# Performance work log

Hardware: AMD Instinct MI355X
Metric: run time of the kernel (lower is better)

Reference implementation:

```python
import jax, jax.numpy as jnp
import numpy as np

B, L, T = 512, 512, 128
START, STOP = T - 2, T - 1   # tag_dict: '<START>'->126, '<STOP>'->127
NEG = -10000.0


def setup_inputs() -> dict:
    key = jax.random.key(0)
    k1, k2, k3, k4 = jax.random.split(key, 4)
    feats = jax.random.normal(k1, (B, L, T), dtype=jnp.float32)
    # learned transition matrix, initialized as in CRF.__init__
    trans = jax.random.normal(k2, (T, T), dtype=jnp.float32)
    trans = trans.at[START, :].set(NEG).at[:, STOP].set(NEG)
    tags = jax.random.randint(k3, (B, L), 0, T - 2)          # gold tags, no START/STOP
    lens = jax.random.randint(k4, (B,), 1, L + 1)            # actual lengths in [1, L]
    return {"feats": feats, "transitions": trans, "tags": tags, "lens": lens}


def _crf_loss(feats, transitions, tags, lens):
    Bn, Ln, Tn = feats.shape

    # ---- forward algorithm (log partition) ----
    init = jnp.full((Tn,), NEG, dtype=feats.dtype).at[START].set(0.0)
    fv0 = jnp.broadcast_to(init, (Bn, Tn))

    def step(fv, xs):
        emit, i = xs                                  # emit: [B, T]
        # tag_var[b, next, prev] = emit[b,next] + trans[next,prev] + fv[b,prev]
        tv = emit[:, :, None] + transitions[None, :, :] + fv[:, None, :]
        new = jax.scipy.special.logsumexp(tv, axis=2)  # [B, T]
        # freeze fv once past each sentence's length (== gathering at index lens)
        fv = jnp.where((i < lens)[:, None], new, fv)
        return fv, None

    fv, _ = jax.lax.scan(step, fv0, (jnp.swapaxes(feats, 0, 1), jnp.arange(Ln)))
    terminal = fv + transitions[START][None, :]       # matches original (uses START row)
    forward_score = jax.scipy.special.logsumexp(terminal, axis=1)  # [B]

    # ---- gold sentence score ----
    start_col = jnp.full((Bn, 1), START, dtype=tags.dtype)
    stop_col = jnp.full((Bn, 1), STOP, dtype=tags.dtype)
    pad_start = jnp.concatenate([start_col, tags], axis=1)   # [B, L+1]
    pad_stop = jnp.concatenate([tags, stop_col], axis=1)     # [B, L+1]
    pos = jnp.arange(Ln + 1)[None, :]
    pad_stop = jnp.where(pos >= lens[:, None], STOP, pad_stop)

    trans_terms = transitions[pad_stop, pad_start]           # [B, L+1]
    trans_sum = jnp.sum(jnp.where(pos <= lens[:, None], trans_terms, 0.0), axis=1)
    emit_terms = jnp.take_along_axis(feats, tags[:, :, None], axis=2)[..., 0]  # [B, L]
    emit_mask = jnp.arange(Ln)[None, :] < lens[:, None]
    emit_sum = jnp.sum(jnp.where(emit_mask, emit_terms, 0.0), axis=1)
    gold_score = trans_sum + emit_sum

    return jnp.mean(forward_score - gold_score)


def reference(feats, transitions, tags, lens):
    return _crf_loss(feats, transitions, tags, lens)
```

## Files before the change

### kernel.cpp

```cpp
#include <hip/hip_runtime.h>

#define Bsz 512
#define Lsz 512
#define Tsz 128
#define TAG_START 126
#define TAG_STOP 127
#define SPB 16
#define UPITCH 136

typedef __attribute__((ext_vector_type(8))) short short8;
typedef __attribute__((ext_vector_type(4))) float f32x4;

__device__ __forceinline__ void lds_barrier() {
  asm volatile("s_waitcnt lgkmcnt(0)\n\ts_barrier" ::: "memory");
}
__device__ __forceinline__ unsigned pack_bf16(float lo, float hi) {
  unsigned a = (__float_as_uint(lo) + 0x8000u) >> 16;
  unsigned b = (__float_as_uint(hi) + 0x8000u) & 0xFFFF0000u;
  return b | a;
}
__device__ __forceinline__ float bf16lo(unsigned d) { return __uint_as_float(d << 16); }
__device__ __forceinline__ float bf16hi(unsigned d) { return __uint_as_float(d & 0xFFFF0000u); }

__global__ __launch_bounds__(256) void crf_fwd_kernel(
    const float* __restrict__ feats, const float* __restrict__ trans,
    const int* __restrict__ tags, const int* __restrict__ lens,
    float* __restrict__ diff_out)
{
  __shared__ __align__(16) unsigned short u_lds[2][SPB][UPITCH];
  __shared__ float red[4][SPB];
  __shared__ float gold_sh[SPB];
  __shared__ int msh;

  const int g    = blockIdx.x;
  const int tid  = threadIdx.x;
  const int w    = tid >> 6;
  const int lane = tid & 63;
  const int q    = lane >> 4;
  const int s    = lane & 15;
  const int seq  = g * SPB + s;
  const int lenc = lens[seq];
  const int lim  = lenc - 1;

  if (tid == 0) msh = 1;
  __syncthreads();
  if (tid < SPB) atomicMax(&msh, lens[g * SPB + tid]);
  for (int i = tid; i < 2 * SPB * UPITCH; i += 256)
    ((unsigned short*)u_lds)[i] = 0;
  __syncthreads();
  const int maxlen = msh;
  if (tid < SPB) u_lds[0][tid][TAG_START] = 0x3F80;
  __syncthreads();

  short8 af[2][4];
  #pragma unroll
  for (int i = 0; i < 2; ++i) {
    const float* tr = trans + (size_t)((2 * w + i) * 16 + s) * Tsz + q * 8;
    #pragma unroll
    for (int c = 0; c < 4; ++c) {
      float4 x = *(const float4*)(tr + c * 32);
      float4 y = *(const float4*)(tr + c * 32 + 4);
      union { unsigned u[4]; short8 v; } cv;
      cv.u[0] = pack_bf16(__expf(x.x), __expf(x.y));
      cv.u[1] = pack_bf16(__expf(x.z), __expf(x.w));
      cv.u[2] = pack_bf16(__expf(y.x), __expf(y.y));
      cv.u[3] = pack_bf16(__expf(y.z), __expf(y.w));
      af[i][c] = cv.v;
    }
  }

  const float* fp0 = feats + (size_t)seq * (Lsz * Tsz) + (2 * w + 0) * 16 + 4 * q;
  const float* fp1 = feats + (size_t)seq * (Lsz * Tsz) + (2 * w + 1) * 16 + 4 * q;

  float4 pa0, pb0, pa1, pb1, pa2, pb2, pa3, pb3;
  { int r1 = (1 < lim) ? 1 : lim, r2 = (2 < lim) ? 2 : lim, r3 = (3 < lim) ? 3 : lim;
    if (lim < 1) r1 = r2 = r3 = lim;
    pa0 = *(const float4*)(fp0);                       pb0 = *(const float4*)(fp1);
    pa1 = *(const float4*)(fp0 + ((size_t)r1 << 7));   pb1 = *(const float4*)(fp1 + ((size_t)r1 << 7));
    pa2 = *(const float4*)(fp0 + ((size_t)r2 << 7));   pb2 = *(const float4*)(fp1 + ((size_t)r2 << 7));
    pa3 = *(const float4*)(fp0 + ((size_t)r3 << 7));   pb3 = *(const float4*)(fp1 + ((size_t)r3 << 7)); }

  float ee[8] = {__expf(pa0.x), __expf(pa0.y), __expf(pa0.z), __expf(pa0.w),
                 __expf(pb0.x), __expf(pb0.y), __expf(pb0.z), __expf(pb0.w)};

  float m_run = 0.0f, mcap = 0.0f;
  float ucap[8];
  #pragma unroll
  for (int i = 0; i < 8; ++i) ucap[i] = 1.0f;

#define STEP(T, PA, PB, NA, NB, BR, BW)                                        \
  { const int t_ = (T);                                                        \
    short8 bq0 = *(const short8*)&u_lds[BR][s][0 * 32 + q * 8];                \
    short8 bq1 = *(const short8*)&u_lds[BR][s][1 * 32 + q * 8];                \
    short8 bq2 = *(const short8*)&u_lds[BR][s][2 * 32 + q * 8];                \
    short8 bq3 = *(const short8*)&u_lds[BR][s][3 * 32 + q * 8];                \
    unsigned ud = *(const unsigned*)&u_lds[BR][s][0];                          \
    int tp = t_ + 4; tp = (tp < lim) ? tp : lim;                               \
    PA = *(const float4*)(fp0 + ((size_t)tp << 7));                            \
    PB = *(const float4*)(fp1 + ((size_t)tp << 7));                            \
    f32x4 acc0 = {0.f, 0.f, 0.f, 0.f}, acc1 = {0.f, 0.f, 0.f, 0.f};            \
    acc0 = __builtin_amdgcn_mfma_f32_16x16x32_bf16(af[0][0], bq0, acc0, 0,0,0);\
    acc1 = __builtin_amdgcn_mfma_f32_16x16x32_bf16(af[1][0], bq0, acc1, 0,0,0);\
    acc0 = __builtin_amdgcn_mfma_f32_16x16x32_bf16(af[0][1], bq1, acc0, 0,0,0);\
    acc1 = __builtin_amdgcn_mfma_f32_16x16x32_bf16(af[1][1], bq1, acc1, 0,0,0);\
    acc0 = __builtin_amdgcn_mfma_f32_16x16x32_bf16(af[0][2], bq2, acc0, 0,0,0);\
    acc1 = __builtin_amdgcn_mfma_f32_16x16x32_bf16(af[1][2], bq2, acc1, 0,0,0);\
    acc0 = __builtin_amdgcn_mfma_f32_16x16x32_bf16(af[0][3], bq3, acc0, 0,0,0);\
    acc1 = __builtin_amdgcn_mfma_f32_16x16x32_bf16(af[1][3], bq3, acc1, 0,0,0);\
    float eta = bf16lo(ud) + bf16hi(ud);                                       \
    if (t_ == 0) eta = 1.0f;                                                   \
    float rce = __builtin_amdgcn_rcpf(eta);                                    \
    bool capt = (t_ == lim);                                                   \
    float uv[8];                                                               \
    _Pragma("unroll") for (int i = 0; i < 4; ++i) {                            \
      uv[i]     = acc0[i] * rce * ee[i];                                       \
      uv[4 + i] = acc1[i] * rce * ee[4 + i];                                   \
    }                                                                          \
    _Pragma("unroll") for (int i = 0; i < 8; ++i)                              \
      ucap[i] = capt ? uv[i] : ucap[i];                                        \
    m_run += __logf(eta);                                                      \
    mcap = capt ? m_run : mcap;                                                \
    unsigned short* dst = &u_lds[BW][s][0];                                    \
    *(unsigned*)&dst[(2 * w + 0) * 16 + 4 * q]     = pack_bf16(uv[0], uv[1]);  \
    *(unsigned*)&dst[(2 * w + 0) * 16 + 4 * q + 2] = pack_bf16(uv[2], uv[3]);  \
    *(unsigned*)&dst[(2 * w + 1) * 16 + 4 * q]     = pack_bf16(uv[4], uv[5]);  \
    *(unsigned*)&dst[(2 * w + 1) * 16 + 4 * q + 2] = pack_bf16(uv[6], uv[7]);  \
    ee[0] = __expf(NA.x); ee[1] = __expf(NA.y);                                \
    ee[2] = __expf(NA.z); ee[3] = __expf(NA.w);                                \
    ee[4] = __expf(NB.x); ee[5] = __expf(NB.y);                                \
    ee[6] = __expf(NB.z); ee[7] = __expf(NB.w);                                \
    lds_barrier();                                                             \
  }

  for (int t = 0; t < maxlen; t += 4) {
    STEP(t + 0, pa0, pb0, pa1, pb1, 0, 1)
    STEP(t + 1, pa1, pb1, pa2, pb2, 1, 0)
    STEP(t + 2, pa2, pb2, pa3, pb3, 0, 1)
    STEP(t + 3, pa3, pb3, pa0, pb0, 1, 0)
  }
#undef STEP

  __syncthreads();

  float fvv[8];
  #pragma unroll
  for (int i = 0; i < 2; ++i)
    #pragma unroll
    for (int r = 0; r < 4; ++r) {
      int row = (2 * w + i) * 16 + 4 * q + r;
      fvv[i * 4 + r] = __logf(ucap[i * 4 + r]) + mcap + trans[TAG_START * Tsz + row];
    }
  float mx = fvv[0];
  #pragma unroll
  for (int i = 1; i < 8; ++i) mx = fmaxf(mx, fvv[i]);
  mx = fmaxf(mx, __shfl_xor(mx, 16, 64));
  mx = fmaxf(mx, __shfl_xor(mx, 32, 64));
  if (q == 0) red[w][s] = mx;
  __syncthreads();
  float gmx = fmaxf(fmaxf(red[0][s], red[1][s]), fmaxf(red[2][s], red[3][s]));
  __syncthreads();
  float se = 0.f;
  #pragma unroll
  for (int i = 0; i < 8; ++i) se += __expf(fvv[i] - gmx);
  se += __shfl_xor(se, 16, 64);
  se += __shfl_xor(se, 32, 64);
  if (q == 0) red[w][s] = se;
  __syncthreads();
  float fwd_score = gmx + __logf((red[0][s] + red[1][s]) + (red[2][s] + red[3][s]));

  {
    int jj = 4 * w + q;
    int gs2 = g * SPB + jj;
    int lenj = lens[gs2];
    const int* tg = tags + (size_t)gs2 * Lsz;
    const float* fbj = feats + (size_t)gs2 * (Lsz * Tsz);
    float acc = 0.f;
    for (int pos = s; pos <= lenj; pos += 16) {
      int st = (pos == 0)    ? TAG_START : tg[pos - 1];
      int et = (pos == lenj) ? TAG_STOP  : tg[pos];
      acc += trans[et * Tsz + st];
    }
    for (int l = s; l < lenj; l += 16)
      acc += fbj[(size_t)l * Tsz + tg[l]];
    #pragma unroll
    for (int off = 1; off < 16; off <<= 1) acc += __shfl_xor(acc, off, 64);
    if (s == 0) gold_sh[jj] = acc;
  }
  __syncthreads();
  if (w == 0 && q == 0)
    diff_out[g * SPB + s] = fwd_score - gold_sh[s];
}

__global__ __launch_bounds__(Bsz) void crf_final_kernel(
    const float* __restrict__ diff, float* __restrict__ out)
{
  int tid = threadIdx.x;
  float v = diff[tid];
  __shared__ float wred[8];
  float sum = v;
  #pragma unroll
  for (int off = 32; off > 0; off >>= 1) sum += __shfl_down(sum, off, 64);
  int wave = tid >> 6, lane = tid & 63;
  if (lane == 0) wred[wave] = sum;
  __syncthreads();
  if (tid == 0) {
    float t = 0.f;
    #pragma unroll
    for (int i = 0; i < 8; ++i) t += wred[i];
    out[0] = t * (1.0f / Bsz);
  }
}

extern "C" void kernel_launch(void* const* d_in, const int* in_sizes, int n_in,
                              void* d_out, int out_size, void* d_ws, size_t ws_size,
                              hipStream_t stream) {
  const float* feats = (const float*)d_in[0];
  const float* trans = (const float*)d_in[1];
  const int*   tags  = (const int*)d_in[2];
  const int*   lens  = (const int*)d_in[3];
  float* out  = (float*)d_out;
  float* diff = (float*)d_ws;

  crf_fwd_kernel<<<Bsz / SPB, 256, 0, stream>>>(feats, trans, tags, lens, diff);
  crf_final_kernel<<<1, Bsz, 0, stream>>>(diff, out);
}
```

Baseline: 406.3 us.

## Split recurrence across eight waves with one 16-row MFMA tile each

Doubles the block to 512 threads so each of eight waves computes one 16-tag output tile per step instead of two, which halves the per-wave MFMA chain, exp work and feature loads on the serial critical path. The final log-sum-exp is reorganized through a shared fv buffer so the original four-wave reduction and gold-score code still run. In exchange, each per-step barrier now synchronizes twice as many waves, and the grid still has only 32 blocks.

```diff
diff --git a/kernel.cpp b/kernel.cpp
--- a/kernel.cpp
+++ b/kernel.cpp
@@ -22,12 +22,13 @@
 __device__ __forceinline__ float bf16lo(unsigned d) { return __uint_as_float(d << 16); }
 __device__ __forceinline__ float bf16hi(unsigned d) { return __uint_as_float(d & 0xFFFF0000u); }
 
-__global__ __launch_bounds__(256) void crf_fwd_kernel(
+__global__ __launch_bounds__(512) void crf_fwd_kernel(
     const float* __restrict__ feats, const float* __restrict__ trans,
     const int* __restrict__ tags, const int* __restrict__ lens,
     float* __restrict__ diff_out)
 {
   __shared__ __align__(16) unsigned short u_lds[2][SPB][UPITCH];
+  __shared__ float fv_sh[Tsz][SPB];
   __shared__ float red[4][SPB];
   __shared__ float gold_sh[SPB];
   __shared__ int msh;
@@ -45,17 +46,16 @@
   if (tid == 0) msh = 1;
   __syncthreads();
   if (tid < SPB) atomicMax(&msh, lens[g * SPB + tid]);
-  for (int i = tid; i < 2 * SPB * UPITCH; i += 256)
+  for (int i = tid; i < 2 * SPB * UPITCH; i += 512)
     ((unsigned short*)u_lds)[i] = 0;
   __syncthreads();
   const int maxlen = msh;
   if (tid < SPB) u_lds[0][tid][TAG_START] = 0x3F80;
   __syncthreads();
 
-  short8 af[2][4];
-  #pragma unroll
-  for (int i = 0; i < 2; ++i) {
-    const float* tr = trans + (size_t)((2 * w + i) * 16 + s) * Tsz + q * 8;
+  short8 af[4];
+  {
+    const float* tr = trans + (size_t)(w * 16 + s) * Tsz + q * 8;
     #pragma unroll
     for (int c = 0; c < 4; ++c) {
       float4 x = *(const float4*)(tr + c * 32);
@@ -65,30 +65,28 @@
       cv.u[1] = pack_bf16(__expf(x.z), __expf(x.w));
       cv.u[2] = pack_bf16(__expf(y.x), __expf(y.y));
       cv.u[3] = pack_bf16(__expf(y.z), __expf(y.w));
-      af[i][c] = cv.v;
+      af[c] = cv.v;
     }
   }
 
-  const float* fp0 = feats + (size_t)seq * (Lsz * Tsz) + (2 * w + 0) * 16 + 4 * q;
-  const float* fp1 = feats + (size_t)seq * (Lsz * Tsz) + (2 * w + 1) * 16 + 4 * q;
-
-  float4 pa0, pb0, pa1, pb1, pa2, pb2, pa3, pb3;
+  const float* fp = feats + (size_t)seq * (Lsz * Tsz) + w * 16 + 4 * q;
+
+  float4 pa0, pa1, pa2, pa3;
   { int r1 = (1 < lim) ? 1 : lim, r2 = (2 < lim) ? 2 : lim, r3 = (3 < lim) ? 3 : lim;
     if (lim < 1) r1 = r2 = r3 = lim;
-    pa0 = *(const float4*)(fp0);                       pb0 = *(const float4*)(fp1);
-    pa1 = *(const float4*)(fp0 + ((size_t)r1 << 7));   pb1 = *(const float4*)(fp1 + ((size_t)r1 << 7));
-    pa2 = *(const float4*)(fp0 + ((size_t)r2 << 7));   pb2 = *(const float4*)(fp1 + ((size_t)r2 << 7));
-    pa3 = *(const float4*)(fp0 + ((size_t)r3 << 7));   pb3 = *(const float4*)(fp1 + ((size_t)r3 << 7)); }
-
-  float ee[8] = {__expf(pa0.x), __expf(pa0.y), __expf(pa0.z), __expf(pa0.w),
-                 __expf(pb0.x), __expf(pb0.y), __expf(pb0.z), __expf(pb0.w)};
+    pa0 = *(const float4*)(fp);
+    pa1 = *(const float4*)(fp + ((size_t)r1 << 7));
+    pa2 = *(const float4*)(fp + ((size_t)r2 << 7));
+    pa3 = *(const float4*)(fp + ((size_t)r3 << 7)); }
+
+  float ee[4] = {__expf(pa0.x), __expf(pa0.y), __expf(pa0.z), __expf(pa0.w)};
 
   float m_run = 0.0f, mcap = 0.0f;
-  float ucap[8];
+  float ucap[4];
   #pragma unroll
-  for (int i = 0; i < 8; ++i) ucap[i] = 1.0f;
-
-#define STEP(T, PA, PB, NA, NB, BR, BW)                                        \
+  for (int i = 0; i < 4; ++i) ucap[i] = 1.0f;
+
+#define STEP(T, PA, NA, BR, BW)                                                \
   { const int t_ = (T);                                                        \
     short8 bq0 = *(const short8*)&u_lds[BR][s][0 * 32 + q * 8];                \
     short8 bq1 = *(const short8*)&u_lds[BR][s][1 * 32 + q * 8];                \
@@ -96,79 +94,80 @@
     short8 bq3 = *(const short8*)&u_lds[BR][s][3 * 32 + q * 8];                \
     unsigned ud = *(const unsigned*)&u_lds[BR][s][0];                          \
     int tp = t_ + 4; tp = (tp < lim) ? tp : lim;                               \
-    PA = *(const float4*)(fp0 + ((size_t)tp << 7));                            \
-    PB = *(const float4*)(fp1 + ((size_t)tp << 7));                            \
-    f32x4 acc0 = {0.f, 0.f, 0.f, 0.f}, acc1 = {0.f, 0.f, 0.f, 0.f};            \
-    acc0 = __builtin_amdgcn_mfma_f32_16x16x32_bf16(af[0][0], bq0, acc0, 0,0,0);\
-    acc1 = __builtin_amdgcn_mfma_f32_16x16x32_bf16(af[1][0], bq0, acc1, 0,0,0);\
-    acc0 = __builtin_amdgcn_mfma_f32_16x16x32_bf16(af[0][1], bq1, acc0, 0,0,0);\
-    acc1 = __builtin_amdgcn_mfma_f32_16x16x32_bf16(af[1][1], bq1, acc1, 0,0,0);\
-    acc0 = __builtin_amdgcn_mfma_f32_16x16x32_bf16(af[0][2], bq2, acc0, 0,0,0);\
-    acc1 = __builtin_amdgcn_mfma_f32_16x16x32_bf16(af[1][2], bq2, acc1, 0,0,0);\
-    acc0 = __builtin_amdgcn_mfma_f32_16x16x32_bf16(af[0][3], bq3, acc0, 0,0,0);\
-    acc1 = __builtin_amdgcn_mfma_f32_16x16x32_bf16(af[1][3], bq3, acc1, 0,0,0);\
+    PA = *(const float4*)(fp + ((size_t)tp << 7));                             \
+    f32x4 acc = {0.f, 0.f, 0.f, 0.f};                                          \
+    acc = __builtin_amdgcn_mfma_f32_16x16x32_bf16(af[0], bq0, acc, 0,0,0);     \
+    acc = __builtin_amdgcn_mfma_f32_16x16x32_bf16(af[1], bq1, acc, 0,0,0);     \
+    acc = __builtin_amdgcn_mfma_f32_16x16x32_bf16(af[2], bq2, acc, 0,0,0);     \
+    acc = __builtin_amdgcn_mfma_f32_16x16x32_bf16(af[3], bq3, acc, 0,0,0);     \
     float eta = bf16lo(ud) + bf16hi(ud);                                       \
     if (t_ == 0) eta = 1.0f;                                                   \
     float rce = __builtin_amdgcn_rcpf(eta);                                    \
     bool capt = (t_ == lim);                                                   \
-    float uv[8];                                                               \
-    _Pragma("unroll") for (int i = 0; i < 4; ++i) {                            \
-      uv[i]     = acc0[i] * rce * ee[i];                                       \
-      uv[4 + i] = acc1[i] * rce * ee[4 + i];                                   \
-    }                                                                          \
-    _Pragma("unroll") for (int i = 0; i < 8; ++i)                              \
+    float uv[4];                                                               \
+    _Pragma("unroll") for (int i = 0; i < 4; ++i)                              \
+      uv[i] = acc[i] * rce * ee[i];                                            \
+    _Pragma("unroll") for (int i = 0; i < 4; ++i)                              \
       ucap[i] = capt ? uv[i] : ucap[i];                                        \
     m_run += __logf(eta);                                                      \
     mcap = capt ? m_run : mcap;                                                \
     unsigned short* dst = &u_lds[BW][s][0];                                    \
-    *(unsigned*)&dst[(2 * w + 0) * 16 + 4 * q]     = pack_bf16(uv[0], uv[1]);  \
-    *(unsigned*)&dst[(2 * w + 0) * 16 + 4 * q + 2] = pack_bf16(uv[2], uv[3]);  \
-    *(unsigned*)&dst[(2 * w + 1) * 16 + 4 * q]     = pack_bf16(uv[4], uv[5]);  \
-    *(unsigned*)&dst[(2 * w + 1) * 16 + 4 * q + 2] = pack_bf16(uv[6], uv[7]);  \
+    uint2 pk; pk.x = pack_bf16(uv[0], uv[1]); pk.y = pack_bf16(uv[2], uv[3]);  \
+    *(uint2*)&dst[w * 16 + 4 * q] = pk;                                        \
     ee[0] = __expf(NA.x); ee[1] = __expf(NA.y);                                \
     ee[2] = __expf(NA.z); ee[3] = __expf(NA.w);                                \
-    ee[4] = __expf(NB.x); ee[5] = __expf(NB.y);                                \
-    ee[6] = __expf(NB.z); ee[7] = __expf(NB.w);                                \
     lds_barrier();                                                             \
   }
 
   for (int t = 0; t < maxlen; t += 4) {
-    STEP(t + 0, pa0, pb0, pa1, pb1, 0, 1)
-    STEP(t + 1, pa1, pb1, pa2, pb2, 1, 0)
-    STEP(t + 2, pa2, pb2, pa3, pb3, 0, 1)
-    STEP(t + 3, pa3, pb3, pa0, pb0, 1, 0)
+    STEP(t + 0, pa0, pa1, 0, 1)
+    STEP(t + 1, pa1, pa2, 1, 0)
+    STEP(t + 2, pa2, pa3, 0, 1)
+    STEP(t + 3, pa3, pa0, 1, 0)
   }
 #undef STEP
 
   __syncthreads();
 
+  #pragma unroll
+  for (int r = 0; r < 4; ++r) {
+    int row = w * 16 + 4 * q + r;
+    fv_sh[row][s] = __logf(ucap[r]) + mcap + trans[TAG_START * Tsz + row];
+  }
+  __syncthreads();
+
+  float fwd_score = 0.f;
   float fvv[8];
-  #pragma unroll
-  for (int i = 0; i < 2; ++i)
-    #pragma unroll
-    for (int r = 0; r < 4; ++r) {
-      int row = (2 * w + i) * 16 + 4 * q + r;
-      fvv[i * 4 + r] = __logf(ucap[i * 4 + r]) + mcap + trans[TAG_START * Tsz + row];
-    }
-  float mx = fvv[0];
-  #pragma unroll
-  for (int i = 1; i < 8; ++i) mx = fmaxf(mx, fvv[i]);
-  mx = fmaxf(mx, __shfl_xor(mx, 16, 64));
-  mx = fmaxf(mx, __shfl_xor(mx, 32, 64));
-  if (q == 0) red[w][s] = mx;
-  __syncthreads();
-  float gmx = fmaxf(fmaxf(red[0][s], red[1][s]), fmaxf(red[2][s], red[3][s]));
-  __syncthreads();
-  float se = 0.f;
-  #pragma unroll
-  for (int i = 0; i < 8; ++i) se += __expf(fvv[i] - gmx);
-  se += __shfl_xor(se, 16, 64);
-  se += __shfl_xor(se, 32, 64);
-  if (q == 0) red[w][s] = se;
-  __syncthreads();
-  float fwd_score = gmx + __logf((red[0][s] + red[1][s]) + (red[2][s] + red[3][s]));
-
-  {
+  if (w < 4) {
+    #pragma unroll
+    for (int i = 0; i < 2; ++i)
+      #pragma unroll
+      for (int r = 0; r < 4; ++r)
+        fvv[i * 4 + r] = fv_sh[(2 * w + i) * 16 + 4 * q + r][s];
+    float mx = fvv[0];
+    #pragma unroll
+    for (int i = 1; i < 8; ++i) mx = fmaxf(mx, fvv[i]);
+    mx = fmaxf(mx, __shfl_xor(mx, 16, 64));
+    mx = fmaxf(mx, __shfl_xor(mx, 32, 64));
+    if (q == 0) red[w][s] = mx;
+  }
+  __syncthreads();
+  float gmx = 0.f;
+  if (w < 4) gmx = fmaxf(fmaxf(red[0][s], red[1][s]), fmaxf(red[2][s], red[3][s]));
+  __syncthreads();
+  if (w < 4) {
+    float se = 0.f;
+    #pragma unroll
+    for (int i = 0; i < 8; ++i) se += __expf(fvv[i] - gmx);
+    se += __shfl_xor(se, 16, 64);
+    se += __shfl_xor(se, 32, 64);
+    if (q == 0) red[w][s] = se;
+  }
+  __syncthreads();
+  if (w < 4)
+    fwd_score = gmx + __logf((red[0][s] + red[1][s]) + (red[2][s] + red[3][s]));
+
+  if (w < 4) {
     int jj = 4 * w + q;
     int gs2 = g * SPB + jj;
     int lenj = lens[gs2];
@@ -221,6 +220,6 @@
   float* out  = (float*)d_out;
   float* diff = (float*)d_ws;
 
-  crf_fwd_kernel<<<Bsz / SPB, 256, 0, stream>>>(feats, trans, tags, lens, diff);
+  crf_fwd_kernel<<<Bsz / SPB, 512, 0, stream>>>(feats, trans, tags, lens, diff);
   crf_final_kernel<<<1, Bsz, 0, stream>>>(diff, out);
 }
```

Measured after the change: 399.5 us. No clear change (-1.7%).
